# Optimization experiments

Measured on AMD Instinct MI355X. Metric: run time of the kernel, lower is better.

The kernel has to match this reference:

```python
import jax, jax.numpy as jnp
import numpy as np

EMBED_DIM = 1024
NUM_HEADS = 16
HEAD_DIM = EMBED_DIM // NUM_HEADS
SCALE = HEAD_DIM ** -0.5


def setup_inputs() -> dict:
    key = jax.random.key(0)
    ks = jax.random.split(key, 5)
    B, S = 4, 2048
    x = jax.random.normal(ks[0], (B, S, EMBED_DIM), dtype=jnp.float32)
    # Dense(embed_dim*3): kernel [D, 3D], bias [3D] (Keras glorot_uniform; use scaled normal)
    w_qkv = jax.random.normal(ks[1], (EMBED_DIM, 3 * EMBED_DIM), dtype=jnp.float32) * (1.0 / np.sqrt(EMBED_DIM))
    b_qkv = jnp.zeros((3 * EMBED_DIM,), dtype=jnp.float32)
    w_proj = jax.random.normal(ks[2], (EMBED_DIM, EMBED_DIM), dtype=jnp.float32) * (1.0 / np.sqrt(EMBED_DIM))
    b_proj = jnp.zeros((EMBED_DIM,), dtype=jnp.float32)
    return {"x": x, "w_qkv": w_qkv, "b_qkv": b_qkv, "w_proj": w_proj, "b_proj": b_proj}


def reference(x, w_qkv, b_qkv, w_proj, b_proj):
    B, S, D = x.shape
    qkv = x @ w_qkv + b_qkv
    qkv = qkv.reshape(B, S, 3, NUM_HEADS, HEAD_DIM)
    qkv = jnp.transpose(qkv, (2, 0, 3, 1, 4))
    q, k, v = qkv[0], qkv[1], qkv[2]
    # scaled dot-product attention (full [B,H,S,S] scores, matching source)
    attn_logits = jnp.einsum('bhqd,bhkd->bhqk', q, k) * SCALE
    attn = jax.nn.softmax(attn_logits, axis=-1)
    context = jnp.einsum('bhqk,bhkd->bhqd', attn, v)
    context = jnp.transpose(context, (0, 2, 1, 3)).reshape(B, S, D)
    out = context @ w_proj + b_proj
    return out
```

## Files before the change

kernel.cpp:

```cpp
#include <hip/hip_runtime.h>

typedef unsigned short u16;
typedef __attribute__((ext_vector_type(8))) short bf16x8;
typedef __attribute__((ext_vector_type(4))) float f32x4;

__device__ __forceinline__ float bf2f(u16 x) {
  union { unsigned u; float f; } v; v.u = ((unsigned)x) << 16; return v.f;
}
__device__ __forceinline__ u16 f2bf(float f) {
  union { float f; unsigned u; } v; v.f = f;
  unsigned r = v.u + 0x7FFFu + ((v.u >> 16) & 1u);
  return (u16)(r >> 16);
}
__device__ __forceinline__ float clampf(float v) {
  return fmaxf(fminf(v, 1.0e4f), -1.0e4f);
}
__device__ __forceinline__ void gll16(const u16* g, u16* l) {
  __builtin_amdgcn_global_load_lds(
      (const __attribute__((address_space(1))) void*)g,
      (__attribute__((address_space(3))) void*)l, 16, 0, 0);
}

__global__ __launch_bounds__(256) void convert_x(
    const float* __restrict__ x, u16* __restrict__ xbf) {
  const int i0 = (blockIdx.x * 256 + threadIdx.x) * 4;
  const float4 v = *(const float4*)(x + i0);
  xbf[i0 + 0] = f2bf(v.x); xbf[i0 + 1] = f2bf(v.y);
  xbf[i0 + 2] = f2bf(v.z); xbf[i0 + 3] = f2bf(v.w);
}

__global__ __launch_bounds__(256) void transpose_f32_bf16(
    const float* __restrict__ in, u16* __restrict__ out, int R, int C) {
  __shared__ u16 tile[32][33];
  const int bc = blockIdx.x * 32, br = blockIdx.y * 32;
  const int tx = threadIdx.x & 31, ty = threadIdx.x >> 5;
  #pragma unroll
  for (int i = ty; i < 32; i += 8)
    tile[i][tx] = f2bf(in[(size_t)(br + i) * C + bc + tx]);
  __syncthreads();
  #pragma unroll
  for (int i = ty; i < 32; i += 8)
    out[(size_t)(bc + i) * R + br + tx] = tile[tx][i];
}

__global__ __launch_bounds__(256) void gemm1_qkv(
    const u16* __restrict__ A, const u16* __restrict__ Bt,
    const float* __restrict__ bias, u16* __restrict__ qk,
    u16* __restrict__ vt, int K) {
  __shared__ u16 As0[128 * 32], As1[128 * 32];
  __shared__ u16 Bs0[128 * 32], Bs1[128 * 32];
  const int tid = threadIdx.x;
  const int m0 = blockIdx.x * 128, n0 = blockIdx.y * 128;
  const int wave = tid >> 6, lane = tid & 63;
  const int quad = lane >> 4, l16 = lane & 15;
  const int wm = (wave >> 1) * 64, wn = (wave & 1) * 64;
  const int sr = (lane >> 2), sp = lane & 3;

  f32x4 acc[4][4] = {};
  const u16* gA = A + (size_t)(m0 + wave * 32 + sr) * K + sp * 8;
  const u16* gB = Bt + (size_t)(n0 + wave * 32 + sr) * K + sp * 8;

  for (int k0 = 0; k0 < K; k0 += 64) {
    #pragma unroll
    for (int t = 0; t < 2; ++t) {
      gll16(gA + (size_t)(t * 16) * K + k0,      &As0[(wave * 32 + t * 16) * 32]);
      gll16(gA + (size_t)(t * 16) * K + k0 + 32, &As1[(wave * 32 + t * 16) * 32]);
      gll16(gB + (size_t)(t * 16) * K + k0,      &Bs0[(wave * 32 + t * 16) * 32]);
      gll16(gB + (size_t)(t * 16) * K + k0 + 32, &Bs1[(wave * 32 + t * 16) * 32]);
    }
    __syncthreads();
    #pragma unroll
    for (int ks = 0; ks < 2; ++ks) {
      const u16* Ah = ks ? As1 : As0;
      const u16* Bh = ks ? Bs1 : Bs0;
      bf16x8 af[4], bfr[4];
      #pragma unroll
      for (int i = 0; i < 4; ++i)
        af[i] = *(const bf16x8*)&Ah[(wm + i * 16 + l16) * 32 + quad * 8];
      #pragma unroll
      for (int j = 0; j < 4; ++j)
        bfr[j] = *(const bf16x8*)&Bh[(wn + j * 16 + l16) * 32 + quad * 8];
      #pragma unroll
      for (int i = 0; i < 4; ++i)
        #pragma unroll
        for (int j = 0; j < 4; ++j)
          acc[i][j] = __builtin_amdgcn_mfma_f32_16x16x32_bf16(af[i], bfr[j], acc[i][j], 0, 0, 0);
    }
    __syncthreads();
  }

  #pragma unroll
  for (int i = 0; i < 4; ++i) {
    const int row = m0 + wm + i * 16 + quad * 4;
    #pragma unroll
    for (int j = 0; j < 4; ++j) {
      const int col = n0 + wn + j * 16 + l16;
      const float bv = bias[col];
      if (col < 2048) {
        #pragma unroll
        for (int r = 0; r < 4; ++r)
          qk[(size_t)(row + r) * 2048 + col] = f2bf(clampf(acc[i][j][r] + bv));
      } else {
        const int d = col & 63;
        const int hh = (col - 2048) >> 6;
        #pragma unroll
        for (int r = 0; r < 4; ++r) {
          const int rr = row + r;
          const int bb = rr >> 11, ss = rr & 2047;
          vt[(size_t)(bb * 16 + hh) * 131072 + d * 2048 + ss] =
              f2bf(clampf(acc[i][j][r] + bv));
        }
      }
    }
  }
}

__global__ __launch_bounds__(256) void gemm2_proj(
    const u16* __restrict__ A, const u16* __restrict__ Bt,
    const float* __restrict__ bias, float* __restrict__ out, int K) {
  __shared__ u16 As0[128 * 32], As1[128 * 32];
  __shared__ u16 Bs0[128 * 32], Bs1[128 * 32];
  const int tid = threadIdx.x;
  const int m0 = blockIdx.x * 128, n0 = blockIdx.y * 128;
  const int wave = tid >> 6, lane = tid & 63;
  const int quad = lane >> 4, l16 = lane & 15;
  const int wm = (wave >> 1) * 64, wn = (wave & 1) * 64;
  const int sr = (lane >> 2), sp = lane & 3;

  f32x4 acc[4][4] = {};
  const u16* gA = A + (size_t)(m0 + wave * 32 + sr) * K + sp * 8;
  const u16* gB = Bt + (size_t)(n0 + wave * 32 + sr) * K + sp * 8;

  for (int k0 = 0; k0 < K; k0 += 64) {
    #pragma unroll
    for (int t = 0; t < 2; ++t) {
      gll16(gA + (size_t)(t * 16) * K + k0,      &As0[(wave * 32 + t * 16) * 32]);
      gll16(gA + (size_t)(t * 16) * K + k0 + 32, &As1[(wave * 32 + t * 16) * 32]);
      gll16(gB + (size_t)(t * 16) * K + k0,      &Bs0[(wave * 32 + t * 16) * 32]);
      gll16(gB + (size_t)(t * 16) * K + k0 + 32, &Bs1[(wave * 32 + t * 16) * 32]);
    }
    __syncthreads();
    #pragma unroll
    for (int ks = 0; ks < 2; ++ks) {
      const u16* Ah = ks ? As1 : As0;
      const u16* Bh = ks ? Bs1 : Bs0;
      bf16x8 af[4], bfr[4];
      #pragma unroll
      for (int i = 0; i < 4; ++i)
        af[i] = *(const bf16x8*)&Ah[(wm + i * 16 + l16) * 32 + quad * 8];
      #pragma unroll
      for (int j = 0; j < 4; ++j)
        bfr[j] = *(const bf16x8*)&Bh[(wn + j * 16 + l16) * 32 + quad * 8];
      #pragma unroll
      for (int i = 0; i < 4; ++i)
        #pragma unroll
        for (int j = 0; j < 4; ++j)
          acc[i][j] = __builtin_amdgcn_mfma_f32_16x16x32_bf16(af[i], bfr[j], acc[i][j], 0, 0, 0);
    }
    __syncthreads();
  }

  #pragma unroll
  for (int i = 0; i < 4; ++i) {
    const int row = m0 + wm + i * 16 + quad * 4;
    #pragma unroll
    for (int j = 0; j < 4; ++j) {
      const int col = n0 + wn + j * 16 + l16;
      const float bv = bias[col];
      #pragma unroll
      for (int r = 0; r < 4; ++r)
        out[(size_t)(row + r) * 1024 + col] = clampf(acc[i][j][r] + bv);
    }
  }
}

__global__ __launch_bounds__(256, 4) void attn_fused(
    const u16* __restrict__ qk, const u16* __restrict__ vt,
    u16* __restrict__ ctx) {
  __shared__ u16 Ks[64][72];
  __shared__ u16 Vs[64][72];
  __shared__ u16 Pl[4][32][72];
  const int bh = blockIdx.x, qt = blockIdx.y;
  const int b = bh >> 4, h = bh & 15;
  const int tid = threadIdx.x;
  const int w = tid >> 6, lane = tid & 63;
  const int quad = lane >> 4, l16 = lane & 15;
  const int qbase = qt * 128 + w * 32;

  const u16* qptr = qk + (size_t)(b * 2048) * 2048 + h * 64;
  bf16x8 qf[2][2];
  #pragma unroll
  for (int i = 0; i < 2; ++i)
    #pragma unroll
    for (int ks = 0; ks < 2; ++ks)
      qf[i][ks] = *(const bf16x8*)(qptr + (size_t)(qbase + i * 16 + l16) * 2048 + ks * 32 + quad * 8);

  const u16* kptr = qk + (size_t)(b * 2048) * 2048 + 1024 + h * 64;
  const u16* vptr = vt + (size_t)bh * 131072;

  const int srow = tid >> 3, scol = (tid & 7) * 8;

  f32x4 o[2][4] = {};
  f32x4 lacc[2] = {};
  const short one = (short)0x3F80;
  const bf16x8 ones = {one, one, one, one, one, one, one, one};
  const float c2 = 0.125f * 1.44269504088896340736f;

  bf16x8 k0 = *(const bf16x8*)(kptr + (size_t)srow * 2048 + scol);
  bf16x8 k1 = *(const bf16x8*)(kptr + (size_t)(srow + 32) * 2048 + scol);
  bf16x8 v0 = *(const bf16x8*)(vptr + (size_t)srow * 2048 + scol);
  bf16x8 v1 = *(const bf16x8*)(vptr + (size_t)(srow + 32) * 2048 + scol);

  for (int kv0 = 0; kv0 < 2048; kv0 += 64) {
    __syncthreads();
    *(bf16x8*)&Ks[srow][scol]      = k0;
    *(bf16x8*)&Ks[srow + 32][scol] = k1;
    *(bf16x8*)&Vs[srow][scol]      = v0;
    *(bf16x8*)&Vs[srow + 32][scol] = v1;
    __syncthreads();
    const int kvn = (kv0 + 64) & 2047;
    k0 = *(const bf16x8*)(kptr + (size_t)(kvn + srow) * 2048 + scol);
    k1 = *(const bf16x8*)(kptr + (size_t)(kvn + srow + 32) * 2048 + scol);
    v0 = *(const bf16x8*)(vptr + (size_t)srow * 2048 + kvn + scol);
    v1 = *(const bf16x8*)(vptr + (size_t)(srow + 32) * 2048 + kvn + scol);

    f32x4 s[2][4] = {};
    #pragma unroll
    for (int jj = 0; jj < 4; ++jj) {
      #pragma unroll
      for (int ks = 0; ks < 2; ++ks) {
        bf16x8 kf = *(const bf16x8*)&Ks[jj * 16 + l16][ks * 32 + quad * 8];
        #pragma unroll
        for (int i = 0; i < 2; ++i)
          s[i][jj] = __builtin_amdgcn_mfma_f32_16x16x32_bf16(qf[i][ks], kf, s[i][jj], 0, 0, 0);
      }
    }
    #pragma unroll
    for (int i = 0; i < 2; ++i)
      #pragma unroll
      for (int jj = 0; jj < 4; ++jj)
        #pragma unroll
        for (int r = 0; r < 4; ++r) {
          const float p = __builtin_amdgcn_exp2f(s[i][jj][r] * c2);
          union { float f; unsigned u; } vv; vv.f = p;
          Pl[w][i * 16 + quad * 4 + r][jj * 16 + l16] = (u16)((vv.u + 0x8000u) >> 16);
        }
    #pragma unroll
    for (int ks = 0; ks < 2; ++ks) {
      bf16x8 af0 = *(const bf16x8*)&Pl[w][l16][ks * 32 + quad * 8];
      bf16x8 af1 = *(const bf16x8*)&Pl[w][16 + l16][ks * 32 + quad * 8];
      lacc[0] = __builtin_amdgcn_mfma_f32_16x16x32_bf16(af0, ones, lacc[0], 0, 0, 0);
      lacc[1] = __builtin_amdgcn_mfma_f32_16x16x32_bf16(af1, ones, lacc[1], 0, 0, 0);
      #pragma unroll
      for (int j = 0; j < 4; ++j) {
        bf16x8 vf = *(const bf16x8*)&Vs[j * 16 + l16][ks * 32 + quad * 8];
        o[0][j] = __builtin_amdgcn_mfma_f32_16x16x32_bf16(af0, vf, o[0][j], 0, 0, 0);
        o[1][j] = __builtin_amdgcn_mfma_f32_16x16x32_bf16(af1, vf, o[1][j], 0, 0, 0);
      }
    }
  }

  u16* cbase = ctx + (size_t)(b * 2048) * 1024 + h * 64;
  #pragma unroll
  for (int i = 0; i < 2; ++i)
    #pragma unroll
    for (int r = 0; r < 4; ++r) {
      const float inv = 1.0f / lacc[i][r];
      const int q = qbase + i * 16 + quad * 4 + r;
      #pragma unroll
      for (int j = 0; j < 4; ++j)
        cbase[(size_t)q * 1024 + j * 16 + l16] = f2bf(o[i][j][r] * inv);
    }
}

extern "C" void kernel_launch(void* const* d_in, const int* in_sizes, int n_in,
                              void* d_out, int out_size, void* d_ws, size_t ws_size,
                              hipStream_t stream) {
  (void)out_size;
  const float *x = nullptr, *wq = nullptr, *bq = nullptr, *wp = nullptr, *bp = nullptr;
  for (int i = 0; i < n_in; ++i) {
    switch (in_sizes[i]) {
      case 8388608: x  = (const float*)d_in[i]; break;
      case 3145728: wq = (const float*)d_in[i]; break;
      case 3072:    bq = (const float*)d_in[i]; break;
      case 1048576: wp = (const float*)d_in[i]; break;
      case 1024:    bp = (const float*)d_in[i]; break;
      default: break;
    }
  }
  if (!x || !wq || !bq || !wp || !bp) {
    x  = (const float*)d_in[0]; wq = (const float*)d_in[1];
    bq = (const float*)d_in[2]; wp = (const float*)d_in[3];
    bp = (const float*)d_in[4];
  }
  float* out = (float*)d_out;

  const size_t NEED = 75497472;
  if (ws_size < NEED) return;

  char* ws = (char*)d_ws;
  u16* qkb = (u16*)(ws);
  u16* vt  = (u16*)(ws + 33554432);
  u16* xbf = (u16*)(ws + 50331648);
  u16* wT1 = (u16*)(ws + 67108864);
  u16* wT2 = (u16*)(ws + 73400320);

  convert_x<<<8192, 256, 0, stream>>>(x, xbf);
  transpose_f32_bf16<<<dim3(96, 32), 256, 0, stream>>>(wq, wT1, 1024, 3072);
  transpose_f32_bf16<<<dim3(32, 32), 256, 0, stream>>>(wp, wT2, 1024, 1024);
  gemm1_qkv<<<dim3(64, 24), 256, 0, stream>>>(xbf, wT1, bq, qkb, vt, 1024);
  attn_fused<<<dim3(64, 16), 256, 0, stream>>>(qkb, vt, xbf );
  gemm2_proj<<<dim3(64, 8), 256, 0, stream>>>(xbf , wT2, bp, out, 1024);
}
```

Before: 291.4 us.

## Double per-wave query rows in attention and XOR-swizzle LDS tiles

Each wave of the attention kernel now handles 64 query rows instead of 32, so every block covers 256 queries and the grid is halved. Each K/V tile loaded into LDS is therefore reused across twice as many queries, and K fragments are held in registers and reused across the four query sub-tiles. The padded LDS arrays are replaced by an XOR-swizzled 64-wide layout to avoid bank conflicts without padding. The cost is more registers and LDS per block (launch bound lowered to 2 blocks per SM), fewer blocks in flight, and therefore lower occupancy.

```diff
diff --git a/kernel.cpp b/kernel.cpp
--- a/kernel.cpp
+++ b/kernel.cpp
@@ -174,23 +174,28 @@
   }
 }
 
-__global__ __launch_bounds__(256, 4) void attn_fused(
+__device__ __forceinline__ int swz(int row, int col) {
+  const int key = (row ^ (row >> 2)) & 7;
+  return row * 64 + (((col >> 3) ^ key) << 3) + (col & 7);
+}
+
+__global__ __launch_bounds__(256, 2) void attn_fused(
     const u16* __restrict__ qk, const u16* __restrict__ vt,
     u16* __restrict__ ctx) {
-  __shared__ u16 Ks[64][72];
-  __shared__ u16 Vs[64][72];
-  __shared__ u16 Pl[4][32][72];
+  __shared__ u16 Ks[64 * 64];
+  __shared__ u16 Vs[64 * 64];
+  __shared__ u16 Pl[4 * 64 * 64];
   const int bh = blockIdx.x, qt = blockIdx.y;
   const int b = bh >> 4, h = bh & 15;
   const int tid = threadIdx.x;
   const int w = tid >> 6, lane = tid & 63;
   const int quad = lane >> 4, l16 = lane & 15;
-  const int qbase = qt * 128 + w * 32;
+  const int qbase = qt * 256 + w * 64;
 
   const u16* qptr = qk + (size_t)(b * 2048) * 2048 + h * 64;
-  bf16x8 qf[2][2];
-  #pragma unroll
-  for (int i = 0; i < 2; ++i)
+  bf16x8 qf[4][2];
+  #pragma unroll
+  for (int i = 0; i < 4; ++i)
     #pragma unroll
     for (int ks = 0; ks < 2; ++ks)
       qf[i][ks] = *(const bf16x8*)(qptr + (size_t)(qbase + i * 16 + l16) * 2048 + ks * 32 + quad * 8);
@@ -199,9 +204,10 @@
   const u16* vptr = vt + (size_t)bh * 131072;
 
   const int srow = tid >> 3, scol = (tid & 7) * 8;
-
-  f32x4 o[2][4] = {};
-  f32x4 lacc[2] = {};
+  u16* Pw = Pl + w * 4096;
+
+  f32x4 o[4][4] = {};
+  f32x4 lacc[4] = {};
   const short one = (short)0x3F80;
   const bf16x8 ones = {one, one, one, one, one, one, one, one};
   const float c2 = 0.125f * 1.44269504088896340736f;
@@ -213,10 +219,10 @@
 
   for (int kv0 = 0; kv0 < 2048; kv0 += 64) {
     __syncthreads();
-    *(bf16x8*)&Ks[srow][scol]      = k0;
-    *(bf16x8*)&Ks[srow + 32][scol] = k1;
-    *(bf16x8*)&Vs[srow][scol]      = v0;
-    *(bf16x8*)&Vs[srow + 32][scol] = v1;
+    *(bf16x8*)&Ks[swz(srow, scol)]      = k0;
+    *(bf16x8*)&Ks[swz(srow + 32, scol)] = k1;
+    *(bf16x8*)&Vs[swz(srow, scol)]      = v0;
+    *(bf16x8*)&Vs[swz(srow + 32, scol)] = v1;
     __syncthreads();
     const int kvn = (kv0 + 64) & 2047;
     k0 = *(const bf16x8*)(kptr + (size_t)(kvn + srow) * 2048 + scol);
@@ -224,45 +230,53 @@
     v0 = *(const bf16x8*)(vptr + (size_t)srow * 2048 + kvn + scol);
     v1 = *(const bf16x8*)(vptr + (size_t)(srow + 32) * 2048 + kvn + scol);
 
-    f32x4 s[2][4] = {};
-    #pragma unroll
-    for (int jj = 0; jj < 4; ++jj) {
-      #pragma unroll
-      for (int ks = 0; ks < 2; ++ks) {
-        bf16x8 kf = *(const bf16x8*)&Ks[jj * 16 + l16][ks * 32 + quad * 8];
-        #pragma unroll
-        for (int i = 0; i < 2; ++i)
-          s[i][jj] = __builtin_amdgcn_mfma_f32_16x16x32_bf16(qf[i][ks], kf, s[i][jj], 0, 0, 0);
+    bf16x8 kf[4][2];
+    #pragma unroll
+    for (int jj = 0; jj < 4; ++jj)
+      #pragma unroll
+      for (int ks = 0; ks < 2; ++ks)
+        kf[jj][ks] = *(const bf16x8*)&Ks[swz(jj * 16 + l16, ks * 32 + quad * 8)];
+
+    #pragma unroll
+    for (int i = 0; i < 4; ++i) {
+      f32x4 s[4] = {};
+      #pragma unroll
+      for (int jj = 0; jj < 4; ++jj) {
+        s[jj] = __builtin_amdgcn_mfma_f32_16x16x32_bf16(qf[i][0], kf[jj][0], s[jj], 0, 0, 0);
+        s[jj] = __builtin_amdgcn_mfma_f32_16x16x32_bf16(qf[i][1], kf[jj][1], s[jj], 0, 0, 0);
       }
-    }
-    #pragma unroll
-    for (int i = 0; i < 2; ++i)
       #pragma unroll
       for (int jj = 0; jj < 4; ++jj)
         #pragma unroll
         for (int r = 0; r < 4; ++r) {
-          const float p = __builtin_amdgcn_exp2f(s[i][jj][r] * c2);
+          const float p = __builtin_amdgcn_exp2f(s[jj][r] * c2);
           union { float f; unsigned u; } vv; vv.f = p;
-          Pl[w][i * 16 + quad * 4 + r][jj * 16 + l16] = (u16)((vv.u + 0x8000u) >> 16);
+          Pw[swz(i * 16 + quad * 4 + r, jj * 16 + l16)] = (u16)((vv.u + 0x8000u) >> 16);
         }
+    }
+
     #pragma unroll
     for (int ks = 0; ks < 2; ++ks) {
-      bf16x8 af0 = *(const bf16x8*)&Pl[w][l16][ks * 32 + quad * 8];
-      bf16x8 af1 = *(const bf16x8*)&Pl[w][16 + l16][ks * 32 + quad * 8];
-      lacc[0] = __builtin_amdgcn_mfma_f32_16x16x32_bf16(af0, ones, lacc[0], 0, 0, 0);
-      lacc[1] = __builtin_amdgcn_mfma_f32_16x16x32_bf16(af1, ones, lacc[1], 0, 0, 0);
+      bf16x8 af[4];
+      #pragma unroll
+      for (int i = 0; i < 4; ++i)
+        af[i] = *(const bf16x8*)&Pw[swz(i * 16 + l16, ks * 32 + quad * 8)];
+      #pragma unroll
+      for (int i = 0; i < 4; ++i)
+        lacc[i] = __builtin_amdgcn_mfma_f32_16x16x32_bf16(af[i], ones, lacc[i], 0, 0, 0);
       #pragma unroll
       for (int j = 0; j < 4; ++j) {
-        bf16x8 vf = *(const bf16x8*)&Vs[j * 16 + l16][ks * 32 + quad * 8];
-        o[0][j] = __builtin_amdgcn_mfma_f32_16x16x32_bf16(af0, vf, o[0][j], 0, 0, 0);
-        o[1][j] = __builtin_amdgcn_mfma_f32_16x16x32_bf16(af1, vf, o[1][j], 0, 0, 0);
+        bf16x8 vf = *(const bf16x8*)&Vs[swz(j * 16 + l16, ks * 32 + quad * 8)];
+        #pragma unroll
+        for (int i = 0; i < 4; ++i)
+          o[i][j] = __builtin_amdgcn_mfma_f32_16x16x32_bf16(af[i], vf, o[i][j], 0, 0, 0);
       }
     }
   }
 
   u16* cbase = ctx + (size_t)(b * 2048) * 1024 + h * 64;
   #pragma unroll
-  for (int i = 0; i < 2; ++i)
+  for (int i = 0; i < 4; ++i)
     #pragma unroll
     for (int r = 0; r < 4; ++r) {
       const float inv = 1.0f / lacc[i][r];
@@ -309,6 +323,6 @@
   transpose_f32_bf16<<<dim3(96, 32), 256, 0, stream>>>(wq, wT1, 1024, 3072);
   transpose_f32_bf16<<<dim3(32, 32), 256, 0, stream>>>(wp, wT2, 1024, 1024);
   gemm1_qkv<<<dim3(64, 24), 256, 0, stream>>>(xbf, wT1, bq, qkb, vt, 1024);
-  attn_fused<<<dim3(64, 16), 256, 0, stream>>>(qkb, vt, xbf );
+  attn_fused<<<dim3(64, 8), 256, 0, stream>>>(qkb, vt, xbf );
   gemm2_proj<<<dim3(64, 8), 256, 0, stream>>>(xbf , wT2, bp, out, 1024);
 }
```

Result: slower. 323.4 us (+11.0%).
